# Kernel tuning notes

Measured on AMD Instinct MI355X. Metric: run time of the kernel, lower is better.

## Reference

```python
import jax, jax.numpy as jnp
import numpy as np

N, K, D, H, DK, DV, L, E = 16384, 16, 128, 8, 16, 16, 2, 32
DFF = 4 * D
EPS = 1e-5


def _ln(x, g, b):
    mu = jnp.mean(x, axis=-1, keepdims=True)
    var = jnp.var(x, axis=-1, keepdims=True)
    return (x - mu) * jax.lax.rsqrt(var + EPS) * g + b


def setup_inputs() -> dict:
    key = jax.random.key(0)
    ks = jax.random.split(key, 20)
    inp = {
        "node_h": jax.random.normal(ks[0], (N, D), jnp.float32),
        "src_idx": jax.random.randint(ks[1], (N, K), 0, N),
        "edge_feat": jax.random.normal(ks[2], (N, K, E), jnp.float32),
        "t": jax.random.uniform(ks[3], (N, K), jnp.float32),
        "t_now": jnp.ones((1,), jnp.float32),
        # params (linear weights stored [in, out])
        "edge_fc_w": jax.random.normal(ks[4], (E, D), jnp.float32) * (2.0 / (E + D)) ** 0.5,
        "edge_fc_b": jnp.zeros((D,), jnp.float32),
        "basis_freq": jnp.asarray(1.0 / 10 ** np.linspace(0, 9, D), jnp.float32),
        "phase": jax.random.normal(ks[5], (D,), jnp.float32),
        "wq": jax.random.normal(ks[6], (L, D, H * DK), jnp.float32) * np.sqrt(2.0 / (D + DK)),
        "wk": jax.random.normal(ks[7], (L, D, H * DK), jnp.float32) * np.sqrt(2.0 / (D + DK)),
        "wv": jax.random.normal(ks[8], (L, D, H * DV), jnp.float32) * np.sqrt(2.0 / (D + DV)),
        "attn_fc_w": jax.random.normal(ks[9], (L, H * DV, D), jnp.float32) * (2.0 / (H * DV + D)) ** 0.5,
        "attn_fc_b": jnp.zeros((L, D), jnp.float32),
        "attn_ln_g": jnp.ones((L, D), jnp.float32),
        "attn_ln_b": jnp.zeros((L, D), jnp.float32),
        "ffn_w1": jax.random.normal(ks[10], (L, D, DFF), jnp.float32) * (1.0 / D) ** 0.5,
        "ffn_b1": jnp.zeros((L, DFF), jnp.float32),
        "ffn_w2": jax.random.normal(ks[11], (L, DFF, D), jnp.float32) * (1.0 / DFF) ** 0.5,
        "ffn_b2": jnp.zeros((L, D), jnp.float32),
        "ffn_ln_g": jnp.ones((L, D), jnp.float32),
        "ffn_ln_b": jnp.zeros((L, D), jnp.float32),
        "fea2node_w": jax.random.normal(ks[12], (D, D), jnp.float32) * (2.0 / (D + D)) ** 0.5,
        "fea2node_b": jnp.zeros((D,), jnp.float32),
        "final_ln_g": jnp.ones((D,), jnp.float32),
        "final_ln_b": jnp.zeros((D,), jnp.float32),
    }
    return inp


def reference(node_h, src_idx, edge_feat, t, t_now,
              edge_fc_w, edge_fc_b, basis_freq, phase,
              wq, wk, wv, attn_fc_w, attn_fc_b, attn_ln_g, attn_ln_b,
              ffn_w1, ffn_b1, ffn_w2, ffn_b2, ffn_ln_g, ffn_ln_b,
              fea2node_w, fea2node_b, final_ln_g, final_ln_b):
    scale = 1.0 / np.sqrt(DK).astype(np.float32)
    # message_func: gather src features, edge transform, temporal encoding
    t_enc = jnp.cos((t_now[0] - t)[..., None] * basis_freq + phase)        # [N,K,D]
    z = node_h[src_idx] + jax.nn.gelu(edge_feat @ edge_fc_w + edge_fc_b) + t_enc
    # reduce_func: inner_layer transformer blocks over the K-neighbor mailbox
    f = z
    for i in range(L):
        q = (f @ wq[i]).reshape(N, K, H, DK)
        k = (f @ wk[i]).reshape(N, K, H, DK)
        v = (f @ wv[i]).reshape(N, K, H, DV)
        attn = jax.nn.softmax(jnp.einsum('nqhd,nkhd->nhqk', q, k) * scale, axis=-1)
        out = jnp.einsum('nhqk,nkhd->nqhd', attn, v).reshape(N, K, H * DV)
        f = _ln(out @ attn_fc_w[i] + attn_fc_b[i] + f, attn_ln_g[i], attn_ln_b[i])
        hid = jax.nn.relu(f @ ffn_w1[i] + ffn_b1[i])                        # [N,K,4D]
        f = _ln(hid @ ffn_w2[i] + ffn_b2[i] + f, ffn_ln_g[i], ffn_ln_b[i])
    pooled = jnp.mean(f, axis=1)                                            # [N,D]
    out = _ln(jax.nn.gelu(pooled @ fea2node_w + fea2node_b) + node_h,
              final_ln_g, final_ln_b)
    return out
```

## Files before the change

### kernel.cpp

```cpp
#include <hip/hip_runtime.h>

#define NN 16384
#define OFF_EWT 0
#define OFF_WQT 4096
#define OFF_WKT 36864
#define OFF_WVT 69632
#define OFF_AFT 102400
#define OFF_W1T 135168
#define OFF_W2T 266240
#define OFF_F2N 397312
#define TOTAL_W 413696

typedef __attribute__((ext_vector_type(8))) short bf16x8;
typedef __attribute__((ext_vector_type(4))) short bf16x4;
typedef __attribute__((ext_vector_type(4))) float f32x4;

static __device__ __forceinline__ short f2bf(float f) {
  unsigned u = __builtin_bit_cast(unsigned, f);
  u += 0x7fffu + ((u >> 16) & 1u);
  return (short)(u >> 16);
}
static __device__ __forceinline__ float bf2f(short h) {
  unsigned u = ((unsigned)(unsigned short)h) << 16;
  return __builtin_bit_cast(float, u);
}
static __device__ __forceinline__ float gelu_f(float x) {
  float e = __expf(1.5957691216057308f * (x + 0.044715f * x * x * x));
  return x - x / (e + 1.0f);
}
static __device__ __forceinline__ f32x4 mfma16(bf16x8 a, bf16x8 b, f32x4 c) {
  return __builtin_amdgcn_mfma_f32_16x16x32_bf16(a, b, c, 0, 0, 0);
}
#define SWZM(row) (((((row) & 7) << 4)) ^ ((((row) >> 3) & 3) << 5))
static __device__ __forceinline__ int swzb(int row, int col) {
  return row * 256 + ((col * 2) ^ SWZM(row));
}
static __device__ __forceinline__ bf16x8 tile_ld8(const short* base, int row, int col) {
  return *(const bf16x8*)((const char*)base + swzb(row, col));
}
static __device__ __forceinline__ void tile_st16(short* base, int row, int col, short v) {
  *(short*)((char*)base + swzb(row, col)) = v;
}
static __device__ __forceinline__ void stage_w(short* dst, const short* src, int stride,
                                               int w, int lane) {
  #pragma unroll
  for (int it = 0; it < 2; ++it) {
    int dbase = (it * 4 + w) * 1024;
    int d = dbase + lane * 16;
    int row = d >> 8;
    int scolb = (d & 255) ^ SWZM(row);
    const short* sp = src + row * stride + (scolb >> 1);
    __builtin_amdgcn_global_load_lds(
        (const __attribute__((address_space(1))) unsigned int*)sp,
        (__attribute__((address_space(3))) unsigned int*)((char*)dst + dbase),
        16, 0, 0);
  }
}

#define LDS_FENCE() do {                                       \
    asm volatile("s_waitcnt lgkmcnt(0)" ::: "memory");         \
    __builtin_amdgcn_sched_barrier(0);                         \
  } while (0)

#define ISSUE(SRC, STRIDE) stage_w(bn, (SRC), (STRIDE), w, lane)
#define ENDSTEP() do {                                         \
    __syncthreads();                                           \
    short* _t = bc; bc = bn; bn = _t;                          \
  } while (0)

#define LD_FA2() do {                                                     \
    _Pragma("unroll") for (int _s = 0; _s < 4; ++_s) {                    \
      fA0[_s] = tile_ld8(myQ0, li, _s * 32 + lq * 8);                     \
      fA1[_s] = tile_ld8(myQ1, li, _s * 32 + lq * 8);                     \
    }                                                                     \
  } while (0)

#define ST_TILE(T, ACC)                                                   \
  _Pragma("unroll") for (int _c = 0; _c < 8; ++_c)                        \
    _Pragma("unroll") for (int _r = 0; _r < 4; ++_r)                      \
      tile_st16((T), lq * 4 + _r, _c * 16 + li, f2bf((ACC)[_c][_r]));

#define PROJ2D(BB)                                                        \
    f32x4 ga0 = F0, ga1 = F0, gb0 = F0, gb1 = F0;                         \
    _Pragma("unroll") for (int _s = 0; _s < 4; ++_s) {                    \
      int _sc = _s * 32 + lq * 8;                                         \
      bf16x8 _b0 = tile_ld8((BB), 0 + li, _sc);                           \
      bf16x8 _b1 = tile_ld8((BB), 16 + li, _sc);                          \
      ga0 = mfma16(fA0[_s], _b0, ga0); gb0 = mfma16(fA1[_s], _b0, gb0);   \
      ga1 = mfma16(fA0[_s], _b1, ga1); gb1 = mfma16(fA1[_s], _b1, gb1);   \
    }

#define ST2D(D0, D1, CB)                                                  \
    _Pragma("unroll") for (int _r = 0; _r < 4; ++_r) {                    \
      tile_st16((D0), lq * 4 + _r, (CB) * 16 + li, f2bf(ga0[_r]));        \
      tile_st16((D0), lq * 4 + _r, ((CB) + 1) * 16 + li, f2bf(ga1[_r]));  \
      tile_st16((D1), lq * 4 + _r, (CB) * 16 + li, f2bf(gb0[_r]));        \
      tile_st16((D1), lq * 4 + _r, ((CB) + 1) * 16 + li, f2bf(gb1[_r]));  \
    }

#define ACC2D(AR0, AR1, CB, BB)                                           \
    _Pragma("unroll") for (int _s = 0; _s < 4; ++_s) {                    \
      int _sc = _s * 32 + lq * 8;                                         \
      bf16x8 _b0 = tile_ld8((BB), 0 + li, _sc);                           \
      bf16x8 _b1 = tile_ld8((BB), 16 + li, _sc);                          \
      acc0[(CB)] = mfma16(AR0[_s], _b0, acc0[(CB)]);                      \
      acc1[(CB)] = mfma16(AR1[_s], _b0, acc1[(CB)]);                      \
      acc0[(CB) + 1] = mfma16(AR0[_s], _b1, acc0[(CB) + 1]);              \
      acc1[(CB) + 1] = mfma16(AR1[_s], _b1, acc1[(CB) + 1]);              \
    }

#define LAYER_NORM(A, GP, BP) do {                                        \
    float _gg[8], _bb[8];                                                 \
    _Pragma("unroll") for (int _c = 0; _c < 8; ++_c) {                    \
      _gg[_c] = (GP)[_c * 16 + li]; _bb[_c] = (BP)[_c * 16 + li]; }       \
    _Pragma("unroll") for (int _r = 0; _r < 4; ++_r) {                    \
      float _s1 = 0.f, _s2 = 0.f;                                         \
      _Pragma("unroll") for (int _c = 0; _c < 8; ++_c) {                  \
        float _v = (A)[_c][_r]; _s1 += _v; _s2 += _v * _v; }              \
      _Pragma("unroll") for (int _m = 1; _m <= 8; _m <<= 1) {             \
        _s1 += __shfl_xor(_s1, _m, 64); _s2 += __shfl_xor(_s2, _m, 64); } \
      float _mean = _s1 * (1.f / 128.f);                                  \
      float _var = _s2 * (1.f / 128.f) - _mean * _mean;                   \
      float _rstd = rsqrtf(_var + 1e-5f);                                 \
      _Pragma("unroll") for (int _c = 0; _c < 8; ++_c)                    \
        (A)[_c][_r] = ((A)[_c][_r] - _mean) * _rstd * _gg[_c] + _bb[_c];  \
    }                                                                     \
  } while (0)

#define ATTN(MYQ, MYK, VACC, OA) do {                                     \
    f32x4 _st[8];                                                         \
    _Pragma("unroll") for (int _h = 0; _h < 8; ++_h) {                    \
      bf16x8 _ka = B0, _qa = B0;                                          \
      if (lq < 2) {                                                       \
        _ka = tile_ld8((MYK), li, _h * 16 + lq * 8);                      \
        _qa = tile_ld8((MYQ), li, _h * 16 + lq * 8);                      \
      }                                                                   \
      _st[_h] = mfma16(_ka, _qa, F0);                                     \
    }                                                                     \
    LDS_FENCE();                                                          \
    _Pragma("unroll") for (int _c = 0; _c < 8; ++_c) {                    \
      bf16x4 _pk;                                                         \
      _Pragma("unroll") for (int _r = 0; _r < 4; ++_r)                    \
        _pk[_r] = f2bf((VACC)[_c][_r]);                                   \
      *(bf16x4*)((MYK) + (_c * 16 + li) * 16 + lq * 4) = _pk;             \
    }                                                                     \
    LDS_FENCE();                                                          \
    _Pragma("unroll") for (int _h = 0; _h < 8; ++_h) {                    \
      float _p[4]; float _mx = -1e30f;                                    \
      _Pragma("unroll") for (int _r = 0; _r < 4; ++_r) {                  \
        _p[_r] = _st[_h][_r] * 0.25f; _mx = fmaxf(_mx, _p[_r]); }         \
      _mx = fmaxf(_mx, __shfl_xor(_mx, 16, 64));                          \
      _mx = fmaxf(_mx, __shfl_xor(_mx, 32, 64));                          \
      float _sum = 0.f;                                                   \
      _Pragma("unroll") for (int _r = 0; _r < 4; ++_r) {                  \
        _p[_r] = __expf(_p[_r] - _mx); _sum += _p[_r]; }                  \
      _sum += __shfl_xor(_sum, 16, 64);                                   \
      _sum += __shfl_xor(_sum, 32, 64);                                   \
      float _inv = 1.0f / _sum;                                           \
      _Pragma("unroll") for (int _r = 0; _r < 4; ++_r) _p[_r] *= _inv;    \
      bf16x8 _pa;                                                         \
      _Pragma("unroll") for (int _j = 0; _j < 8; ++_j) {                  \
        float _v = __shfl(_p[_j & 3], li + 16 * (2 * lq + (_j >> 2)), 64);\
        _pa[_j] = (lq < 2) ? f2bf(_v) : (short)0;                         \
      }                                                                   \
      bf16x8 _vb = B0;                                                    \
      if (lq < 2) _vb = *(const bf16x8*)((MYK) + (_h * 16 + li) * 16 + lq * 8); \
      f32x4 _o = mfma16(_pa, _vb, F0);                                    \
      _Pragma("unroll") for (int _r = 0; _r < 4; ++_r)                    \
        tile_st16((MYQ), lq * 4 + _r, _h * 16 + li, f2bf(_o[_r]));        \
    }                                                                     \
    LDS_FENCE();                                                          \
    _Pragma("unroll") for (int _s = 0; _s < 4; ++_s)                      \
      (OA)[_s] = tile_ld8((MYQ), li, _s * 32 + lq * 8);                   \
  } while (0)

__global__ void prep_kernel(const float* __restrict__ ew, const float* __restrict__ wq,
                            const float* __restrict__ wk, const float* __restrict__ wv,
                            const float* __restrict__ afc, const float* __restrict__ w1,
                            const float* __restrict__ w2, const float* __restrict__ f2n,
                            short* __restrict__ wsb) {
  int tt = blockIdx.x * 256 + threadIdx.x;
  if (tt >= TOTAL_W) return;
  short v;
  if (tt < OFF_WQT) {
    int u = tt; int row = u >> 5, colr = u & 31;
    v = f2bf(ew[colr * 128 + row]);
  } else if (tt < OFF_WKT) {
    int u = tt - OFF_WQT; int i = u >> 14; u &= 16383; int row = u >> 7, colr = u & 127;
    v = f2bf(wq[i * 16384 + colr * 128 + row]);
  } else if (tt < OFF_WVT) {
    int u = tt - OFF_WKT; int i = u >> 14; u &= 16383; int row = u >> 7, colr = u & 127;
    v = f2bf(wk[i * 16384 + colr * 128 + row]);
  } else if (tt < OFF_AFT) {
    int u = tt - OFF_WVT; int i = u >> 14; u &= 16383; int row = u >> 7, colr = u & 127;
    v = f2bf(wv[i * 16384 + colr * 128 + row]);
  } else if (tt < OFF_W1T) {
    int u = tt - OFF_AFT; int i = u >> 14; u &= 16383; int row = u >> 7, colr = u & 127;
    v = f2bf(afc[i * 16384 + colr * 128 + row]);
  } else if (tt < OFF_W2T) {
    int u = tt - OFF_W1T; int i = u >> 16; u &= 65535; int row = u >> 7, colr = u & 127;
    v = f2bf(w1[i * 65536 + colr * 512 + row]);
  } else if (tt < OFF_F2N) {
    int u = tt - OFF_W2T; int i = u >> 16; u &= 65535; int row = u >> 9, colr = u & 511;
    v = f2bf(w2[i * 65536 + colr * 128 + row]);
  } else {
    int u = tt - OFF_F2N; int row = u >> 7, colr = u & 127;
    v = f2bf(f2n[colr * 128 + row]);
  }
  wsb[tt] = v;
}

__global__ __launch_bounds__(256, 2) void fused_kernel(
    const float* __restrict__ node_h, const int* __restrict__ src_idx,
    const float* __restrict__ edge_feat, const float* __restrict__ t_arr,
    const float* __restrict__ t_now, const float* __restrict__ edge_fc_b,
    const float* __restrict__ basis_freq, const float* __restrict__ phase,
    const float* __restrict__ attn_fc_b, const float* __restrict__ attn_ln_g,
    const float* __restrict__ attn_ln_b, const float* __restrict__ ffn_b1,
    const float* __restrict__ ffn_b2, const float* __restrict__ ffn_ln_g,
    const float* __restrict__ ffn_ln_b, const float* __restrict__ f2n_b,
    const float* __restrict__ fin_g, const float* __restrict__ fin_b,
    const short* __restrict__ wsb, float* __restrict__ out) {
  __shared__ __align__(16) short bufs0[4096];
  __shared__ __align__(16) short bufs1[4096];
  __shared__ __align__(16) short lds_qk[4][8192];

  const int tid = (int)threadIdx.x;
  const int w = tid >> 6, lane = tid & 63, li = lane & 15, lq = lane >> 4;
  const int n0 = (int)blockIdx.x * 8 + w * 2;
  const int n1 = n0 + 1;
  short* myQ0 = lds_qk[w];
  short* myK0 = lds_qk[w] + 2048;
  short* myQ1 = lds_qk[w] + 4096;
  short* myK1 = lds_qk[w] + 6144;
  short* bc = bufs0;
  short* bn = bufs1;
  const f32x4 F0 = {0.f, 0.f, 0.f, 0.f};
  const bf16x8 B0 = {0, 0, 0, 0, 0, 0, 0, 0};

  stage_w(bc, wsb + OFF_WQT, 128, w, lane);

  const float tnow = t_now[0];

  f32x4 acc0[8], acc1[8];
  {
    const short* ewt = wsb + OFF_EWT;
    const float* ef0 = edge_feat + ((size_t)(n0 * 16 + li)) * 32 + lq * 8;
    const float* ef1 = edge_feat + ((size_t)(n1 * 16 + li)) * 32 + lq * 8;
    f32x4 ea0 = *(const f32x4*)(ef0), ea0b = *(const f32x4*)(ef0 + 4);
    f32x4 ea1 = *(const f32x4*)(ef1), ea1b = *(const f32x4*)(ef1 + 4);
    bf16x8 e0, e1;
    #pragma unroll
    for (int j = 0; j < 4; ++j) {
      e0[j] = f2bf(ea0[j]); e0[j + 4] = f2bf(ea0b[j]);
      e1[j] = f2bf(ea1[j]); e1[j + 4] = f2bf(ea1b[j]);
    }
    #pragma unroll
    for (int c = 0; c < 8; ++c) {
      bf16x8 eb = *(const bf16x8*)(ewt + (c * 16 + li) * 32 + lq * 8);
      acc0[c] = mfma16(e0, eb, F0);
      acc1[c] = mfma16(e1, eb, F0);
    }
  }
  {
    float bfq[8], phs[8], ebs[8];
    #pragma unroll
    for (int c = 0; c < 8; ++c) {
      int col = c * 16 + li;
      bfq[c] = basis_freq[col]; phs[c] = phase[col]; ebs[c] = edge_fc_b[col];
    }
    #pragma unroll
    for (int r = 0; r < 4; ++r) {
      int m = lq * 4 + r;
      int s0 = src_idx[n0 * 16 + m], s1 = src_idx[n1 * 16 + m];
      float dt0 = tnow - t_arr[n0 * 16 + m], dt1 = tnow - t_arr[n1 * 16 + m];
      const float* nh0 = node_h + (size_t)s0 * 128;
      const float* nh1 = node_h + (size_t)s1 * 128;
      #pragma unroll
      for (int c = 0; c < 8; ++c) {
        int col = c * 16 + li;
        acc0[c][r] = gelu_f(acc0[c][r] + ebs[c]) + nh0[col] + __cosf(dt0 * bfq[c] + phs[c]);
        acc1[c][r] = gelu_f(acc1[c][r] + ebs[c]) + nh1[col] + __cosf(dt1 * bfq[c] + phs[c]);
      }
    }
  }
  ST_TILE(myQ0, acc0);
  ST_TILE(myQ1, acc1);
  __syncthreads();

  bf16x8 fA0[4], fA1[4];
  bf16x8 oa0_[4], oa1_[4];
  bf16x8 ha0_[4], ha1_[4];

  for (int il = 0; il < 2; ++il) {
    const short* WQT = wsb + OFF_WQT + il * 16384;
    const short* WKT = wsb + OFF_WKT + il * 16384;
    const short* WVT = wsb + OFF_WVT + il * 16384;
    const short* AFT = wsb + OFF_AFT + il * 16384;
    const short* W1T = wsb + OFF_W1T + il * 65536;
    const short* W2T = wsb + OFF_W2T + il * 65536;
    const short* WQN = wsb + OFF_WQT + ((il == 0) ? 16384 : 0);

    f32x4 vacc0[8], vacc1[8];

    #pragma unroll
    for (int q = 0; q < 4; ++q) {
      const short* nx = (q < 3) ? (WQT + (q + 1) * 4096) : WKT;
      ISSUE(nx, 128);
      if (q == 0) LD_FA2();
      { PROJ2D(bc); ST2D(myQ0, myQ1, q * 2); }
      ENDSTEP();
    }
    #pragma unroll
    for (int q = 0; q < 4; ++q) {
      const short* nx = (q < 3) ? (WKT + (q + 1) * 4096) : WVT;
      ISSUE(nx, 128);
      { PROJ2D(bc); ST2D(myK0, myK1, q * 2); }
      ENDSTEP();
    }
    #pragma unroll
    for (int q = 0; q < 4; ++q) {
      const short* nx = (q < 3) ? (WVT + (q + 1) * 4096) : AFT;
      ISSUE(nx, 128);
      {
        PROJ2D(bc);
        vacc0[q * 2] = ga0; vacc0[q * 2 + 1] = ga1;
        vacc1[q * 2] = gb0; vacc1[q * 2 + 1] = gb1;
      }
      if (q == 3) {
        ATTN(myQ0, myK0, vacc0, oa0_);
        ATTN(myQ1, myK1, vacc1, oa1_);
      }
      ENDSTEP();
    }
    #pragma unroll
    for (int q = 0; q < 4; ++q) {
      const short* nx = (q < 3) ? (AFT + (q + 1) * 4096) : W1T;
      ISSUE(nx, 128);
      #pragma unroll
      for (int j = 0; j < 2; ++j) {
        float b = attn_fc_b[il * 128 + (q * 2 + j) * 16 + li];
        #pragma unroll
        for (int r = 0; r < 4; ++r) { acc0[q * 2 + j][r] += b; acc1[q * 2 + j][r] += b; }
      }
      ACC2D(oa0_, oa1_, q * 2, bc);
      if (q == 3) {
        LAYER_NORM(acc0, attn_ln_g + il * 128, attn_ln_b + il * 128);
        LAYER_NORM(acc1, attn_ln_g + il * 128, attn_ln_b + il * 128);
        ST_TILE(myQ0, acc0);
        ST_TILE(myQ1, acc1);
        LD_FA2();
        #pragma unroll
        for (int c = 0; c < 8; ++c) {
          float b2 = ffn_b2[il * 128 + c * 16 + li];
          #pragma unroll
          for (int r = 0; r < 4; ++r) { acc0[c][r] += b2; acc1[c][r] += b2; }
        }
      }
      ENDSTEP();
    }

    for (int ct = 0; ct < 4; ++ct) {
      const short* W1c = W1T + ct * 16384;
      const short* W2c = W2T + ct * 128;
      const float* b1p = ffn_b1 + il * 512 + ct * 128;
      #pragma unroll
      for (int q = 0; q < 4; ++q) {
        const short* nx = (q < 3) ? (W1c + (q + 1) * 4096) : W2c;
        ISSUE(nx, (q < 3) ? 128 : 512);
        {
          PROJ2D(bc);
          float ba = b1p[(q * 2) * 16 + li], bb = b1p[(q * 2 + 1) * 16 + li];
          #pragma unroll
          for (int r = 0; r < 4; ++r) {
            tile_st16(myK0, lq * 4 + r, (q * 2) * 16 + li, f2bf(fmaxf(ga0[r] + ba, 0.f)));
            tile_st16(myK0, lq * 4 + r, (q * 2 + 1) * 16 + li, f2bf(fmaxf(ga1[r] + bb, 0.f)));
            tile_st16(myK1, lq * 4 + r, (q * 2) * 16 + li, f2bf(fmaxf(gb0[r] + ba, 0.f)));
            tile_st16(myK1, lq * 4 + r, (q * 2 + 1) * 16 + li, f2bf(fmaxf(gb1[r] + bb, 0.f)));
          }
        }
        if (q == 3) {
          LDS_FENCE();
          #pragma unroll
          for (int s = 0; s < 4; ++s) {
            ha0_[s] = tile_ld8(myK0, li, s * 32 + lq * 8);
            ha1_[s] = tile_ld8(myK1, li, s * 32 + lq * 8);
          }
        }
        ENDSTEP();
      }
      #pragma unroll
      for (int q = 0; q < 4; ++q) {
        const short* nx;
        int nstr;
        if (q < 3) { nx = W2c + (q + 1) * 32 * 512; nstr = 512; }
        else if (ct < 3) { nx = W1T + (ct + 1) * 16384; nstr = 128; }
        else { nx = WQN; nstr = 128; }
        ISSUE(nx, nstr);
        ACC2D(ha0_, ha1_, q * 2, bc);
        if (ct == 3 && q == 3) {
          LAYER_NORM(acc0, ffn_ln_g + il * 128, ffn_ln_b + il * 128);
          LAYER_NORM(acc1, ffn_ln_g + il * 128, ffn_ln_b + il * 128);
          ST_TILE(myQ0, acc0);
          ST_TILE(myQ1, acc1);
        }
        ENDSTEP();
      }
    }
  }
  asm volatile("s_waitcnt vmcnt(0)" ::: "memory");

  {
    float pc0[8], pc1[8];
    #pragma unroll
    for (int c = 0; c < 8; ++c) {
      float s0 = acc0[c][0] + acc0[c][1] + acc0[c][2] + acc0[c][3];
      float s1 = acc1[c][0] + acc1[c][1] + acc1[c][2] + acc1[c][3];
      s0 += __shfl_xor(s0, 16, 64); s0 += __shfl_xor(s0, 32, 64);
      s1 += __shfl_xor(s1, 16, 64); s1 += __shfl_xor(s1, 32, 64);
      pc0[c] = s0 * (1.f / 16.f);
      pc1[c] = s1 * (1.f / 16.f);
    }
    float* ps0 = (float*)myK0;
    float* ps1 = (float*)myK1;
    if (lq == 0) {
      #pragma unroll
      for (int c = 0; c < 8; ++c) { ps0[c * 16 + li] = pc0[c]; ps1[c * 16 + li] = pc1[c]; }
    }
    LDS_FENCE();
    const short* F2NT = wsb + OFF_F2N;
    #pragma unroll
    for (int nd = 0; nd < 2; ++nd) {
      const float* ps = nd ? ps1 : ps0;
      int n = nd ? n1 : n0;
      float yv[2];
      #pragma unroll
      for (int half = 0; half < 2; ++half) {
        int col = half * 64 + lane;
        float dot = 0.f;
        for (int d0 = 0; d0 < 128; d0 += 8) {
          bf16x8 wv8 = *(const bf16x8*)(F2NT + col * 128 + d0);
          f32x4 p0 = *(const f32x4*)(ps + d0);
          f32x4 p1 = *(const f32x4*)(ps + d0 + 4);
          dot += p0[0] * bf2f(wv8[0]) + p0[1] * bf2f(wv8[1]) + p0[2] * bf2f(wv8[2]) + p0[3] * bf2f(wv8[3]);
          dot += p1[0] * bf2f(wv8[4]) + p1[1] * bf2f(wv8[5]) + p1[2] * bf2f(wv8[6]) + p1[3] * bf2f(wv8[7]);
        }
        yv[half] = gelu_f(dot + f2n_b[col]) + node_h[(size_t)n * 128 + col];
      }
      float s1v = yv[0] + yv[1], s2v = yv[0] * yv[0] + yv[1] * yv[1];
      #pragma unroll
      for (int m = 1; m <= 32; m <<= 1) {
        s1v += __shfl_xor(s1v, m, 64); s2v += __shfl_xor(s2v, m, 64);
      }
      float mean = s1v * (1.f / 128.f);
      float var = s2v * (1.f / 128.f) - mean * mean;
      float rstd = rsqrtf(var + 1e-5f);
      #pragma unroll
      for (int half = 0; half < 2; ++half) {
        int col = half * 64 + lane;
        out[(size_t)n * 128 + col] = (yv[half] - mean) * rstd * fin_g[col] + fin_b[col];
      }
    }
  }
}

extern "C" void kernel_launch(void* const* d_in, const int* in_sizes, int n_in,
                              void* d_out, int out_size, void* d_ws, size_t ws_size,
                              hipStream_t stream) {
  const float* node_h    = (const float*)d_in[0];
  const int*   src_idx   = (const int*)d_in[1];
  const float* edge_feat = (const float*)d_in[2];
  const float* t_arr     = (const float*)d_in[3];
  const float* t_now     = (const float*)d_in[4];
  const float* edge_fc_w = (const float*)d_in[5];
  const float* edge_fc_b = (const float*)d_in[6];
  const float* basis_frq = (const float*)d_in[7];
  const float* phase     = (const float*)d_in[8];
  const float* wq        = (const float*)d_in[9];
  const float* wk        = (const float*)d_in[10];
  const float* wv        = (const float*)d_in[11];
  const float* attn_fc_w = (const float*)d_in[12];
  const float* attn_fc_b = (const float*)d_in[13];
  const float* attn_ln_g = (const float*)d_in[14];
  const float* attn_ln_b = (const float*)d_in[15];
  const float* ffn_w1    = (const float*)d_in[16];
  const float* ffn_b1    = (const float*)d_in[17];
  const float* ffn_w2    = (const float*)d_in[18];
  const float* ffn_b2    = (const float*)d_in[19];
  const float* ffn_ln_g  = (const float*)d_in[20];
  const float* ffn_ln_b  = (const float*)d_in[21];
  const float* f2n_w     = (const float*)d_in[22];
  const float* f2n_b     = (const float*)d_in[23];
  const float* fin_g     = (const float*)d_in[24];
  const float* fin_b     = (const float*)d_in[25];
  short* wsb = (short*)d_ws;

  prep_kernel<<<(TOTAL_W + 255) / 256, 256, 0, stream>>>(
      edge_fc_w, wq, wk, wv, attn_fc_w, ffn_w1, ffn_w2, f2n_w, wsb);
  fused_kernel<<<NN / 8, 256, 0, stream>>>(
      node_h, src_idx, edge_feat, t_arr, t_now, edge_fc_b, basis_frq, phase,
      attn_fc_b, attn_ln_g, attn_ln_b, ffn_b1, ffn_b2, ffn_ln_g, ffn_ln_b,
      f2n_b, fin_g, fin_b, wsb, (float*)d_out);
}
```

Baseline: 689.7 us.

## Replace LDS-staged double-buffered weights with direct global loads in one-wave blocks

Removes the cooperative LDS weight staging (global_load_lds double buffering plus block barriers) and has each single-wave block read bf16 weight fragments straight from global memory or cache into MFMA operands. Blocks shrink to 64 threads handling 2 nodes, so the grid grows fourfold and the LDS per block drops. The change removes __syncthreads and staging overhead but makes every wave fetch the full weight set through the cache hierarchy, with no sharing across waves. Q/K/V projection for the two nodes is now done one node at a time, which halves weight reuse per load.

Result: slower. 1.535 ms (+122.6%).

```diff
diff --git a/kernel.cpp b/kernel.cpp
--- a/kernel.cpp
+++ b/kernel.cpp
@@ -41,20 +41,8 @@
 static __device__ __forceinline__ void tile_st16(short* base, int row, int col, short v) {
   *(short*)((char*)base + swzb(row, col)) = v;
 }
-static __device__ __forceinline__ void stage_w(short* dst, const short* src, int stride,
-                                               int w, int lane) {
-  #pragma unroll
-  for (int it = 0; it < 2; ++it) {
-    int dbase = (it * 4 + w) * 1024;
-    int d = dbase + lane * 16;
-    int row = d >> 8;
-    int scolb = (d & 255) ^ SWZM(row);
-    const short* sp = src + row * stride + (scolb >> 1);
-    __builtin_amdgcn_global_load_lds(
-        (const __attribute__((address_space(1))) unsigned int*)sp,
-        (__attribute__((address_space(3))) unsigned int*)((char*)dst + dbase),
-        16, 0, 0);
-  }
+static __device__ __forceinline__ bf16x8 gld8(const short* W, int row, int col, int stride) {
+  return *(const bf16x8*)(W + row * stride + col);
 }
 
 #define LDS_FENCE() do {                                       \
@@ -62,52 +50,27 @@
     __builtin_amdgcn_sched_barrier(0);                         \
   } while (0)
 
-#define ISSUE(SRC, STRIDE) stage_w(bn, (SRC), (STRIDE), w, lane)
-#define ENDSTEP() do {                                         \
-    __syncthreads();                                           \
-    short* _t = bc; bc = bn; bn = _t;                          \
-  } while (0)
-
-#define LD_FA2() do {                                                     \
-    _Pragma("unroll") for (int _s = 0; _s < 4; ++_s) {                    \
-      fA0[_s] = tile_ld8(myQ0, li, _s * 32 + lq * 8);                     \
-      fA1[_s] = tile_ld8(myQ1, li, _s * 32 + lq * 8);                     \
-    }                                                                     \
-  } while (0)
-
 #define ST_TILE(T, ACC)                                                   \
   _Pragma("unroll") for (int _c = 0; _c < 8; ++_c)                        \
     _Pragma("unroll") for (int _r = 0; _r < 4; ++_r)                      \
       tile_st16((T), lq * 4 + _r, _c * 16 + li, f2bf((ACC)[_c][_r]));
 
-#define PROJ2D(BB)                                                        \
-    f32x4 ga0 = F0, ga1 = F0, gb0 = F0, gb1 = F0;                         \
-    _Pragma("unroll") for (int _s = 0; _s < 4; ++_s) {                    \
-      int _sc = _s * 32 + lq * 8;                                         \
-      bf16x8 _b0 = tile_ld8((BB), 0 + li, _sc);                           \
-      bf16x8 _b1 = tile_ld8((BB), 16 + li, _sc);                          \
-      ga0 = mfma16(fA0[_s], _b0, ga0); gb0 = mfma16(fA1[_s], _b0, gb0);   \
-      ga1 = mfma16(fA0[_s], _b1, ga1); gb1 = mfma16(fA1[_s], _b1, gb1);   \
-    }
-
-#define ST2D(D0, D1, CB)                                                  \
-    _Pragma("unroll") for (int _r = 0; _r < 4; ++_r) {                    \
-      tile_st16((D0), lq * 4 + _r, (CB) * 16 + li, f2bf(ga0[_r]));        \
-      tile_st16((D0), lq * 4 + _r, ((CB) + 1) * 16 + li, f2bf(ga1[_r]));  \
-      tile_st16((D1), lq * 4 + _r, (CB) * 16 + li, f2bf(gb0[_r]));        \
-      tile_st16((D1), lq * 4 + _r, ((CB) + 1) * 16 + li, f2bf(gb1[_r]));  \
-    }
-
-#define ACC2D(AR0, AR1, CB, BB)                                           \
-    _Pragma("unroll") for (int _s = 0; _s < 4; ++_s) {                    \
-      int _sc = _s * 32 + lq * 8;                                         \
-      bf16x8 _b0 = tile_ld8((BB), 0 + li, _sc);                           \
-      bf16x8 _b1 = tile_ld8((BB), 16 + li, _sc);                          \
-      acc0[(CB)] = mfma16(AR0[_s], _b0, acc0[(CB)]);                      \
-      acc1[(CB)] = mfma16(AR1[_s], _b0, acc1[(CB)]);                      \
-      acc0[(CB) + 1] = mfma16(AR0[_s], _b1, acc0[(CB) + 1]);              \
-      acc1[(CB) + 1] = mfma16(AR1[_s], _b1, acc1[(CB) + 1]);              \
-    }
+#define PROJ_SOLO_ST(WB, FA, DST)                                         \
+  _Pragma("unroll") for (int _c = 0; _c < 8; ++_c) {                      \
+    f32x4 _g = F0;                                                        \
+    _Pragma("unroll") for (int _s = 0; _s < 4; ++_s)                      \
+      _g = mfma16((FA)[_s], gld8((WB), _c * 16 + li, _s * 32 + lq * 8, 128), _g); \
+    _Pragma("unroll") for (int _r = 0; _r < 4; ++_r)                      \
+      tile_st16((DST), lq * 4 + _r, _c * 16 + li, f2bf(_g[_r]));          \
+  }
+
+#define PROJ_SOLO_V(WB, FA, VACC)                                         \
+  _Pragma("unroll") for (int _c = 0; _c < 8; ++_c) {                      \
+    f32x4 _g = F0;                                                        \
+    _Pragma("unroll") for (int _s = 0; _s < 4; ++_s)                      \
+      _g = mfma16((FA)[_s], gld8((WB), _c * 16 + li, _s * 32 + lq * 8, 128), _g); \
+    (VACC)[_c] = _g;                                                      \
+  }
 
 #define LAYER_NORM(A, GP, BP) do {                                        \
     float _gg[8], _bb[8];                                                 \
@@ -172,6 +135,7 @@
     LDS_FENCE();                                                          \
     _Pragma("unroll") for (int _s = 0; _s < 4; ++_s)                      \
       (OA)[_s] = tile_ld8((MYQ), li, _s * 32 + lq * 8);                   \
+    LDS_FENCE();                                                          \
   } while (0)
 
 __global__ void prep_kernel(const float* __restrict__ ew, const float* __restrict__ wq,
@@ -210,7 +174,7 @@
   wsb[tt] = v;
 }
 
-__global__ __launch_bounds__(256, 2) void fused_kernel(
+__global__ __launch_bounds__(64, 3) void fused_kernel(
     const float* __restrict__ node_h, const int* __restrict__ src_idx,
     const float* __restrict__ edge_feat, const float* __restrict__ t_arr,
     const float* __restrict__ t_now, const float* __restrict__ edge_fc_b,
@@ -221,24 +185,17 @@
     const float* __restrict__ ffn_ln_b, const float* __restrict__ f2n_b,
     const float* __restrict__ fin_g, const float* __restrict__ fin_b,
     const short* __restrict__ wsb, float* __restrict__ out) {
-  __shared__ __align__(16) short bufs0[4096];
-  __shared__ __align__(16) short bufs1[4096];
-  __shared__ __align__(16) short lds_qk[4][8192];
-
-  const int tid = (int)threadIdx.x;
-  const int w = tid >> 6, lane = tid & 63, li = lane & 15, lq = lane >> 4;
-  const int n0 = (int)blockIdx.x * 8 + w * 2;
+  __shared__ __align__(16) short fT[2][2048];
+  __shared__ __align__(16) short scr[4096];
+
+  const int lane = (int)threadIdx.x;
+  const int li = lane & 15, lq = lane >> 4;
+  const int n0 = (int)blockIdx.x * 2;
   const int n1 = n0 + 1;
-  short* myQ0 = lds_qk[w];
-  short* myK0 = lds_qk[w] + 2048;
-  short* myQ1 = lds_qk[w] + 4096;
-  short* myK1 = lds_qk[w] + 6144;
-  short* bc = bufs0;
-  short* bn = bufs1;
+  short* scrQ = scr;
+  short* scrK = scr + 2048;
   const f32x4 F0 = {0.f, 0.f, 0.f, 0.f};
   const bf16x8 B0 = {0, 0, 0, 0, 0, 0, 0, 0};
-
-  stage_w(bc, wsb + OFF_WQT, 128, w, lane);
 
   const float tnow = t_now[0];
 
@@ -284,9 +241,9 @@
       }
     }
   }
-  ST_TILE(myQ0, acc0);
-  ST_TILE(myQ1, acc1);
-  __syncthreads();
+  ST_TILE(fT[0], acc0);
+  ST_TILE(fT[1], acc1);
+  LDS_FENCE();
 
   bf16x8 fA0[4], fA1[4];
   bf16x8 oa0_[4], oa1_[4];
@@ -299,116 +256,103 @@
     const short* AFT = wsb + OFF_AFT + il * 16384;
     const short* W1T = wsb + OFF_W1T + il * 65536;
     const short* W2T = wsb + OFF_W2T + il * 65536;
-    const short* WQN = wsb + OFF_WQT + ((il == 0) ? 16384 : 0);
-
-    f32x4 vacc0[8], vacc1[8];
-
-    #pragma unroll
-    for (int q = 0; q < 4; ++q) {
-      const short* nx = (q < 3) ? (WQT + (q + 1) * 4096) : WKT;
-      ISSUE(nx, 128);
-      if (q == 0) LD_FA2();
-      { PROJ2D(bc); ST2D(myQ0, myQ1, q * 2); }
-      ENDSTEP();
-    }
-    #pragma unroll
-    for (int q = 0; q < 4; ++q) {
-      const short* nx = (q < 3) ? (WKT + (q + 1) * 4096) : WVT;
-      ISSUE(nx, 128);
-      { PROJ2D(bc); ST2D(myK0, myK1, q * 2); }
-      ENDSTEP();
-    }
-    #pragma unroll
-    for (int q = 0; q < 4; ++q) {
-      const short* nx = (q < 3) ? (WVT + (q + 1) * 4096) : AFT;
-      ISSUE(nx, 128);
-      {
-        PROJ2D(bc);
-        vacc0[q * 2] = ga0; vacc0[q * 2 + 1] = ga1;
-        vacc1[q * 2] = gb0; vacc1[q * 2 + 1] = gb1;
-      }
-      if (q == 3) {
-        ATTN(myQ0, myK0, vacc0, oa0_);
-        ATTN(myQ1, myK1, vacc1, oa1_);
-      }
-      ENDSTEP();
-    }
-    #pragma unroll
-    for (int q = 0; q < 4; ++q) {
-      const short* nx = (q < 3) ? (AFT + (q + 1) * 4096) : W1T;
-      ISSUE(nx, 128);
-      #pragma unroll
-      for (int j = 0; j < 2; ++j) {
-        float b = attn_fc_b[il * 128 + (q * 2 + j) * 16 + li];
+
+    #pragma unroll
+    for (int s = 0; s < 4; ++s) fA0[s] = tile_ld8(fT[0], li, s * 32 + lq * 8);
+    {
+      f32x4 vacc[8];
+      PROJ_SOLO_ST(WQT, fA0, scrQ);
+      PROJ_SOLO_ST(WKT, fA0, scrK);
+      PROJ_SOLO_V(WVT, fA0, vacc);
+      LDS_FENCE();
+      ATTN(scrQ, scrK, vacc, oa0_);
+    }
+    #pragma unroll
+    for (int s = 0; s < 4; ++s) fA1[s] = tile_ld8(fT[1], li, s * 32 + lq * 8);
+    {
+      f32x4 vacc[8];
+      PROJ_SOLO_ST(WQT, fA1, scrQ);
+      PROJ_SOLO_ST(WKT, fA1, scrK);
+      PROJ_SOLO_V(WVT, fA1, vacc);
+      LDS_FENCE();
+      ATTN(scrQ, scrK, vacc, oa1_);
+    }
+
+    #pragma unroll
+    for (int c = 0; c < 8; ++c) {
+      float b = attn_fc_b[il * 128 + c * 16 + li];
+      #pragma unroll
+      for (int r = 0; r < 4; ++r) { acc0[c][r] += b; acc1[c][r] += b; }
+    }
+    #pragma unroll
+    for (int c = 0; c < 8; ++c) {
+      #pragma unroll
+      for (int s = 0; s < 4; ++s) {
+        bf16x8 b = gld8(AFT, c * 16 + li, s * 32 + lq * 8, 128);
+        acc0[c] = mfma16(oa0_[s], b, acc0[c]);
+        acc1[c] = mfma16(oa1_[s], b, acc1[c]);
+      }
+    }
+    LAYER_NORM(acc0, attn_ln_g + il * 128, attn_ln_b + il * 128);
+    LAYER_NORM(acc1, attn_ln_g + il * 128, attn_ln_b + il * 128);
+    ST_TILE(fT[0], acc0);
+    ST_TILE(fT[1], acc1);
+    LDS_FENCE();
+    #pragma unroll
+    for (int s = 0; s < 4; ++s) {
+      fA0[s] = tile_ld8(fT[0], li, s * 32 + lq * 8);
+      fA1[s] = tile_ld8(fT[1], li, s * 32 + lq * 8);
+    }
+    #pragma unroll
+    for (int c = 0; c < 8; ++c) {
+      float b2 = ffn_b2[il * 128 + c * 16 + li];
+      #pragma unroll
+      for (int r = 0; r < 4; ++r) { acc0[c][r] += b2; acc1[c][r] += b2; }
+    }
+
+    for (int ct = 0; ct < 4; ++ct) {
+      const short* W1B = W1T + ct * 128 * 128;
+      const short* W2B = W2T + ct * 128;
+      const float* b1p = ffn_b1 + il * 512 + ct * 128;
+      LDS_FENCE();
+      #pragma unroll
+      for (int cc = 0; cc < 8; ++cc) {
+        f32x4 g0 = F0, g1 = F0;
         #pragma unroll
-        for (int r = 0; r < 4; ++r) { acc0[q * 2 + j][r] += b; acc1[q * 2 + j][r] += b; }
-      }
-      ACC2D(oa0_, oa1_, q * 2, bc);
-      if (q == 3) {
-        LAYER_NORM(acc0, attn_ln_g + il * 128, attn_ln_b + il * 128);
-        LAYER_NORM(acc1, attn_ln_g + il * 128, attn_ln_b + il * 128);
-        ST_TILE(myQ0, acc0);
-        ST_TILE(myQ1, acc1);
-        LD_FA2();
+        for (int s = 0; s < 4; ++s) {
+          bf16x8 b = gld8(W1B, cc * 16 + li, s * 32 + lq * 8, 128);
+          g0 = mfma16(fA0[s], b, g0);
+          g1 = mfma16(fA1[s], b, g1);
+        }
+        float b1 = b1p[cc * 16 + li];
         #pragma unroll
-        for (int c = 0; c < 8; ++c) {
-          float b2 = ffn_b2[il * 128 + c * 16 + li];
-          #pragma unroll
-          for (int r = 0; r < 4; ++r) { acc0[c][r] += b2; acc1[c][r] += b2; }
+        for (int r = 0; r < 4; ++r) {
+          tile_st16(scrQ, lq * 4 + r, cc * 16 + li, f2bf(fmaxf(g0[r] + b1, 0.f)));
+          tile_st16(scrK, lq * 4 + r, cc * 16 + li, f2bf(fmaxf(g1[r] + b1, 0.f)));
         }
       }
-      ENDSTEP();
-    }
-
-    for (int ct = 0; ct < 4; ++ct) {
-      const short* W1c = W1T + ct * 16384;
-      const short* W2c = W2T + ct * 128;
-      const float* b1p = ffn_b1 + il * 512 + ct * 128;
-      #pragma unroll
-      for (int q = 0; q < 4; ++q) {
-        const short* nx = (q < 3) ? (W1c + (q + 1) * 4096) : W2c;
-        ISSUE(nx, (q < 3) ? 128 : 512);
-        {
-          PROJ2D(bc);
-          float ba = b1p[(q * 2) * 16 + li], bb = b1p[(q * 2 + 1) * 16 + li];
-          #pragma unroll
-          for (int r = 0; r < 4; ++r) {
-            tile_st16(myK0, lq * 4 + r, (q * 2) * 16 + li, f2bf(fmaxf(ga0[r] + ba, 0.f)));
-            tile_st16(myK0, lq * 4 + r, (q * 2 + 1) * 16 + li, f2bf(fmaxf(ga1[r] + bb, 0.f)));
-            tile_st16(myK1, lq * 4 + r, (q * 2) * 16 + li, f2bf(fmaxf(gb0[r] + ba, 0.f)));
-            tile_st16(myK1, lq * 4 + r, (q * 2 + 1) * 16 + li, f2bf(fmaxf(gb1[r] + bb, 0.f)));
-          }
+      LDS_FENCE();
+      #pragma unroll
+      for (int s = 0; s < 4; ++s) {
+        ha0_[s] = tile_ld8(scrQ, li, s * 32 + lq * 8);
+        ha1_[s] = tile_ld8(scrK, li, s * 32 + lq * 8);
+      }
+      #pragma unroll
+      for (int c = 0; c < 8; ++c) {
+        #pragma unroll
+        for (int s = 0; s < 4; ++s) {
+          bf16x8 b = gld8(W2B, c * 16 + li, s * 32 + lq * 8, 512);
+          acc0[c] = mfma16(ha0_[s], b, acc0[c]);
+          acc1[c] = mfma16(ha1_[s], b, acc1[c]);
         }
-        if (q == 3) {
-          LDS_FENCE();
-          #pragma unroll
-          for (int s = 0; s < 4; ++s) {
-            ha0_[s] = tile_ld8(myK0, li, s * 32 + lq * 8);
-            ha1_[s] = tile_ld8(myK1, li, s * 32 + lq * 8);
-          }
-        }
-        ENDSTEP();
-      }
-      #pragma unroll
-      for (int q = 0; q < 4; ++q) {
-        const short* nx;
-        int nstr;
-        if (q < 3) { nx = W2c + (q + 1) * 32 * 512; nstr = 512; }
-        else if (ct < 3) { nx = W1T + (ct + 1) * 16384; nstr = 128; }
-        else { nx = WQN; nstr = 128; }
-        ISSUE(nx, nstr);
-        ACC2D(ha0_, ha1_, q * 2, bc);
-        if (ct == 3 && q == 3) {
-          LAYER_NORM(acc0, ffn_ln_g + il * 128, ffn_ln_b + il * 128);
-          LAYER_NORM(acc1, ffn_ln_g + il * 128, ffn_ln_b + il * 128);
-          ST_TILE(myQ0, acc0);
-          ST_TILE(myQ1, acc1);
-        }
-        ENDSTEP();
-      }
-    }
-  }
-  asm volatile("s_waitcnt vmcnt(0)" ::: "memory");
+      }
+    }
+    LAYER_NORM(acc0, ffn_ln_g + il * 128, ffn_ln_b + il * 128);
+    LAYER_NORM(acc1, ffn_ln_g + il * 128, ffn_ln_b + il * 128);
+    ST_TILE(fT[0], acc0);
+    ST_TILE(fT[1], acc1);
+    LDS_FENCE();
+  }
 
   {
     float pc0[8], pc1[8];
@@ -421,8 +365,8 @@
       pc0[c] = s0 * (1.f / 16.f);
       pc1[c] = s1 * (1.f / 16.f);
     }
-    float* ps0 = (float*)myK0;
-    float* ps1 = (float*)myK1;
+    float* ps0 = (float*)scrQ;
+    float* ps1 = (float*)scrK;
     if (lq == 0) {
       #pragma unroll
       for (int c = 0; c < 8; ++c) { ps0[c * 16 + li] = pc0[c]; ps1[c * 16 + li] = pc1[c]; }
@@ -497,7 +441,7 @@
 
   prep_kernel<<<(TOTAL_W + 255) / 256, 256, 0, stream>>>(
       edge_fc_w, wq, wk, wv, attn_fc_w, ffn_w1, ffn_w2, f2n_w, wsb);
-  fused_kernel<<<NN / 8, 256, 0, stream>>>(
+  fused_kernel<<<NN / 2, 64, 0, stream>>>(
       node_h, src_idx, edge_feat, t_arr, t_now, edge_fc_b, basis_frq, phase,
       attn_fc_b, attn_ln_g, attn_ln_b, ffn_b1, ffn_b2, ffn_ln_g, ffn_ln_b,
       f2n_b, fin_g, fin_b, wsb, (float*)d_out);
```

## Split attention into softmax-before-V and PV phases to drop V register accumulators

Applied to the files above, without the earlier changes.

Attention is split into two phases. The QK^T softmax now runs right after the K projection and writes bf16 probabilities into the Q tile in LDS. Each V projection chunk is stored straight to LDS in transposed form instead of being held in 16 f32x4 registers, and a second phase reads the probabilities back and does the PV products. This lowers register pressure and may let softmax overlap better with V projection, at the cost of extra LDS traffic and fences.

Measured after the change: 708.3 us. +2.7%, slower.

```diff
diff --git a/kernel.cpp b/kernel.cpp
--- a/kernel.cpp
+++ b/kernel.cpp
@@ -97,6 +97,12 @@
       tile_st16((D1), lq * 4 + _r, (CB) * 16 + li, f2bf(gb0[_r]));        \
       tile_st16((D1), lq * 4 + _r, ((CB) + 1) * 16 + li, f2bf(gb1[_r]));  \
     }
+
+#define ST_VT(DST, G, CT) do {                                            \
+    bf16x4 _pk;                                                           \
+    _Pragma("unroll") for (int _r = 0; _r < 4; ++_r) _pk[_r] = f2bf((G)[_r]); \
+    *(bf16x4*)((DST) + ((CT) * 16 + li) * 16 + lq * 4) = _pk;             \
+  } while (0)
 
 #define ACC2D(AR0, AR1, CB, BB)                                           \
     _Pragma("unroll") for (int _s = 0; _s < 4; ++_s) {                    \
@@ -127,7 +133,7 @@
     }                                                                     \
   } while (0)
 
-#define ATTN(MYQ, MYK, VACC, OA) do {                                     \
+#define ATTN_SM(MYQ, MYK) do {                                            \
     f32x4 _st[8];                                                         \
     _Pragma("unroll") for (int _h = 0; _h < 8; ++_h) {                    \
       bf16x8 _ka = B0, _qa = B0;                                          \
@@ -136,13 +142,6 @@
         _qa = tile_ld8((MYQ), li, _h * 16 + lq * 8);                      \
       }                                                                   \
       _st[_h] = mfma16(_ka, _qa, F0);                                     \
-    }                                                                     \
-    LDS_FENCE();                                                          \
-    _Pragma("unroll") for (int _c = 0; _c < 8; ++_c) {                    \
-      bf16x4 _pk;                                                         \
-      _Pragma("unroll") for (int _r = 0; _r < 4; ++_r)                    \
-        _pk[_r] = f2bf((VACC)[_c][_r]);                                   \
-      *(bf16x4*)((MYK) + (_c * 16 + li) * 16 + lq * 4) = _pk;             \
     }                                                                     \
     LDS_FENCE();                                                          \
     _Pragma("unroll") for (int _h = 0; _h < 8; ++_h) {                    \
@@ -163,9 +162,20 @@
         float _v = __shfl(_p[_j & 3], li + 16 * (2 * lq + (_j >> 2)), 64);\
         _pa[_j] = (lq < 2) ? f2bf(_v) : (short)0;                         \
       }                                                                   \
+      if (lq < 2)                                                         \
+        *(bf16x8*)((MYQ) + (_h * 32 + lq * 16 + li) * 8) = _pa;           \
+    }                                                                     \
+  } while (0)
+
+#define ATTN_PV(MYQ, MYK, OA) do {                                        \
+    bf16x8 _par[8];                                                       \
+    _Pragma("unroll") for (int _h = 0; _h < 8; ++_h)                      \
+      _par[_h] = (lq < 2) ? *(const bf16x8*)((MYQ) + (_h * 32 + lq * 16 + li) * 8) : B0; \
+    LDS_FENCE();                                                          \
+    _Pragma("unroll") for (int _h = 0; _h < 8; ++_h) {                    \
       bf16x8 _vb = B0;                                                    \
       if (lq < 2) _vb = *(const bf16x8*)((MYK) + (_h * 16 + li) * 16 + lq * 8); \
-      f32x4 _o = mfma16(_pa, _vb, F0);                                    \
+      f32x4 _o = mfma16(_par[_h], _vb, F0);                               \
       _Pragma("unroll") for (int _r = 0; _r < 4; ++_r)                    \
         tile_st16((MYQ), lq * 4 + _r, _h * 16 + li, f2bf(_o[_r]));        \
     }                                                                     \
@@ -301,8 +311,6 @@
     const short* W2T = wsb + OFF_W2T + il * 65536;
     const short* WQN = wsb + OFF_WQT + ((il == 0) ? 16384 : 0);
 
-    f32x4 vacc0[8], vacc1[8];
-
     #pragma unroll
     for (int q = 0; q < 4; ++q) {
       const short* nx = (q < 3) ? (WQT + (q + 1) * 4096) : WKT;
@@ -316,6 +324,12 @@
       const short* nx = (q < 3) ? (WKT + (q + 1) * 4096) : WVT;
       ISSUE(nx, 128);
       { PROJ2D(bc); ST2D(myK0, myK1, q * 2); }
+      if (q == 3) {
+        LDS_FENCE();
+        ATTN_SM(myQ0, myK0);
+        ATTN_SM(myQ1, myK1);
+        LDS_FENCE();
+      }
       ENDSTEP();
     }
     #pragma unroll
@@ -324,12 +338,13 @@
       ISSUE(nx, 128);
       {
         PROJ2D(bc);
-        vacc0[q * 2] = ga0; vacc0[q * 2 + 1] = ga1;
-        vacc1[q * 2] = gb0; vacc1[q * 2 + 1] = gb1;
+        ST_VT(myK0, ga0, q * 2); ST_VT(myK0, ga1, q * 2 + 1);
+        ST_VT(myK1, gb0, q * 2); ST_VT(myK1, gb1, q * 2 + 1);
       }
       if (q == 3) {
-        ATTN(myQ0, myK0, vacc0, oa0_);
-        ATTN(myQ1, myK1, vacc1, oa1_);
+        LDS_FENCE();
+        ATTN_PV(myQ0, myK0, oa0_);
+        ATTN_PV(myQ1, myK1, oa1_);
       }
       ENDSTEP();
     }
```
